# Performance work log

Measured on AMD Instinct MI355X. Metric: run time of the kernel, lower is better.

## Reference

```python
import jax, jax.numpy as jnp
import numpy as np

N, E, B = 10000, 100000, 64
IN_DIM, EDGE_DIM = 16, 8
HID = [32, 64]
OUT_DIM = 128
BN_EPS = 1e-5


def setup_inputs() -> dict:
    key = jax.random.key(0)
    ks = iter(jax.random.split(key, 32))
    inp = {}
    inp["x"] = jax.random.normal(next(ks), (N, IN_DIM), dtype=jnp.float32)
    inp["edge_index"] = jax.random.randint(next(ks), (2, E), 0, N, dtype=jnp.int64)
    inp["edge_attr"] = jax.random.normal(next(ks), (E, EDGE_DIM), dtype=jnp.float32)
    inp["batch"] = jnp.sort(jax.random.randint(next(ks), (N,), 0, B, dtype=jnp.int64))
    inp["edge_batch"] = jax.random.randint(next(ks), (E,), 0, B, dtype=jnp.int64)
    pre = IN_DIM
    for i, hd in enumerate(HID):
        s = 1.0 / np.sqrt(EDGE_DIM)
        inp[f"w_nn{i}"] = jax.random.uniform(next(ks), (pre * hd, EDGE_DIM), jnp.float32, -s, s)
        inp[f"b_nn{i}"] = jax.random.uniform(next(ks), (pre * hd,), jnp.float32, -s, s)
        inp[f"root{i}"] = jax.random.normal(next(ks), (pre, hd), dtype=jnp.float32) / np.sqrt(pre)
        inp[f"bias{i}"] = jnp.zeros((hd,), dtype=jnp.float32)
        inp[f"gamma{i}"] = jnp.ones((hd,), dtype=jnp.float32)
        inp[f"beta{i}"] = jnp.zeros((hd,), dtype=jnp.float32)
        pre = hd
    s = 1.0 / np.sqrt(pre)
    inp["s_w"] = jax.random.uniform(next(ks), (OUT_DIM, pre), jnp.float32, -s, s)
    inp["s_b"] = jax.random.uniform(next(ks), (OUT_DIM,), jnp.float32, -s, s)
    inp["t_w"] = jax.random.uniform(next(ks), (OUT_DIM, pre), jnp.float32, -s, s)
    inp["t_b"] = jax.random.uniform(next(ks), (OUT_DIM,), jnp.float32, -s, s)
    return inp


def _nnconv(x, edge_index, edge_attr, w_nn, b_nn, root, bias, out_dim):
    src, dst = edge_index[0], edge_index[1]
    # per-edge weight matrices [E, in_dim, out_dim]
    W = (edge_attr @ w_nn.T + b_nn).reshape(edge_attr.shape[0], -1, out_dim)
    msg = jnp.einsum('ei,eio->eo', x[src], W)  # gather + per-edge matmul
    agg = jax.ops.segment_sum(msg, dst, num_segments=N)  # scatter-add
    return agg + x @ root + bias


def _bn(x, gamma, beta):
    mu = jnp.mean(x, axis=0)
    var = jnp.mean((x - mu) ** 2, axis=0)  # biased var (torch BN training)
    return gamma * (x - mu) * jax.lax.rsqrt(var + BN_EPS) + beta


def reference(x, edge_index, edge_attr, batch, edge_batch,
              w_nn0, b_nn0, root0, bias0, gamma0, beta0,
              w_nn1, b_nn1, root1, bias1, gamma1, beta1,
              s_w, s_b, t_w, t_b):
    x = jax.nn.relu(_bn(_nnconv(x, edge_index, edge_attr, w_nn0, b_nn0, root0, bias0, HID[0]), gamma0, beta0))
    x = jax.nn.relu(_bn(_nnconv(x, edge_index, edge_attr, w_nn1, b_nn1, root1, bias1, HID[1]), gamma1, beta1))
    s_x = jnp.clip(x @ s_w.T + s_b, -30.0, 30.0)
    t_x = x @ t_w.T + t_b
    f_x = jax.nn.sigmoid(-s_x) * jnp.tanh(t_x)  # 1/(1+exp(s)) == sigmoid(-s)
    return jax.ops.segment_sum(f_x, batch, num_segments=B)
```

## Files before the change

### kernel.cpp

```cpp
#include <hip/hip_runtime.h>
#include <math.h>

#define NN 10000
#define NE 100000
#define BN_EPS 1e-5f

__global__ __launch_bounds__(256) void k_prep(
    const float* __restrict__ w0, const float* __restrict__ b0,
    const float* __restrict__ root0,
    const float* __restrict__ w1, const float* __restrict__ b1,
    const float* __restrict__ root1,
    const float* __restrict__ s_w, const float* __restrict__ t_w,
    float* __restrict__ wT0, float* __restrict__ wT1, float* __restrict__ wstT,
    float* __restrict__ st0, float* __restrict__ st1, float* __restrict__ out)
{
  int gid = blockIdx.x * 256 + threadIdx.x;
  int gsz = gridDim.x * 256;
  for (int idx = gid; idx < 16 * 320; idx += gsz) {
    int i = idx / 320, c = idx - i * 320;
    float v;
    if (c < 256)      v = w0[(i * 32 + (c & 31)) * 8 + (c >> 5)];
    else if (c < 288) v = b0[i * 32 + (c - 256)];
    else              v = root0[i * 32 + (c - 288)];
    wT0[idx] = v;
  }
  for (int idx = gid; idx < 32 * 640; idx += gsz) {
    int i = idx / 640, c = idx - i * 640;
    float v;
    if (c < 512)      v = w1[(i * 64 + (c & 63)) * 8 + (c >> 6)];
    else if (c < 576) v = b1[i * 64 + (c - 512)];
    else              v = root1[i * 64 + (c - 576)];
    wT1[idx] = v;
  }
  for (int idx = gid; idx < 64 * 256; idx += gsz) {
    int i = idx >> 8, o = idx & 255;
    wstT[idx] = (o < 128) ? s_w[o * 64 + i] : t_w[(o - 128) * 64 + i];
  }
  for (int idx = gid; idx < 64 * 128; idx += gsz) out[idx] = 0.f;
  if (gid < 64)  st0[gid] = 0.f;
  if (gid < 128) st1[gid] = 0.f;
}

__global__ __launch_bounds__(320) void k_node0(
    const float* __restrict__ x, const float* __restrict__ wT0,
    const float* __restrict__ bias0,
    float* __restrict__ G0, float* __restrict__ h0)
{
  int c = threadIdx.x;
  float wc[16];
#pragma unroll
  for (int i = 0; i < 16; ++i) wc[i] = wT0[i * 320 + c];
  float bi = (c >= 288) ? bias0[c - 288] : 0.f;

  int n0 = blockIdx.x * 20;
  for (int n = n0; n < n0 + 20; n += 2) {
    const float4* xa = (const float4*)(x + n * 16);
    float a0 = 0.f, a1 = 0.f;
#pragma unroll
    for (int q = 0; q < 4; ++q) {
      float4 v0 = xa[q], v1 = xa[q + 4];
      a0 = fmaf(v0.x, wc[4 * q + 0], a0); a1 = fmaf(v1.x, wc[4 * q + 0], a1);
      a0 = fmaf(v0.y, wc[4 * q + 1], a0); a1 = fmaf(v1.y, wc[4 * q + 1], a1);
      a0 = fmaf(v0.z, wc[4 * q + 2], a0); a1 = fmaf(v1.z, wc[4 * q + 2], a1);
      a0 = fmaf(v0.w, wc[4 * q + 3], a0); a1 = fmaf(v1.w, wc[4 * q + 3], a1);
    }
    if (c < 288) {
      G0[n * 288 + c]       = a0;
      G0[(n + 1) * 288 + c] = a1;
    } else {
      h0[n * 32 + (c - 288)]       = a0 + bi;
      h0[(n + 1) * 32 + (c - 288)] = a1 + bi;
    }
  }
}

__global__ __launch_bounds__(256) void k_edge0(
    const int* __restrict__ ei, const float* __restrict__ ea,
    const float* __restrict__ G0, float* __restrict__ h0)
{
  int tid = threadIdx.x;
  int e = blockIdx.x * 8 + (tid >> 5);
  if (e >= NE) return;
  int o = tid & 31;
  int src = ei[e], dst = ei[NE + e];
  const float* gr = G0 + src * 288;
  const float* er = ea + e * 8;
  float m = gr[256 + o];
#pragma unroll
  for (int k = 0; k < 8; ++k) m = fmaf(er[k], gr[k * 32 + o], m);
  unsafeAtomicAdd(&h0[dst * 32 + o], m);
}

template <int C>
__global__ __launch_bounds__(256) void k_stats(
    const float* __restrict__ h, float* __restrict__ st)
{
  const int RPB = 256 / C;
  int tid = threadIdx.x;
  int col = tid % C, rg = tid / C;
  float s1 = 0.f, s2 = 0.f;
  int step = gridDim.x * RPB;
  for (int n = blockIdx.x * RPB + rg; n < NN; n += step) {
    float v = h[n * C + col];
    s1 += v; s2 += v * v;
  }
  __shared__ float l1[256], l2[256];
  l1[tid] = s1; l2[tid] = s2;
  __syncthreads();
  if (tid < C) {
    for (int r = 1; r < RPB; ++r) { s1 += l1[r * C + tid]; s2 += l2[r * C + tid]; }
    unsafeAtomicAdd(&st[tid], s1);
    unsafeAtomicAdd(&st[C + tid], s2);
  }
}

__global__ __launch_bounds__(256) void k_x1(
    float* __restrict__ h0, const float* __restrict__ st0,
    const float* __restrict__ g0, const float* __restrict__ be0)
{
  __shared__ float sc[32], sh[32];
  int tid = threadIdx.x;
  if (tid < 32) {
    float mu  = st0[tid] * (1.0f / NN);
    float var = st0[32 + tid] * (1.0f / NN) - mu * mu;
    float s   = g0[tid] * rsqrtf(var + BN_EPS);
    sc[tid] = s;
    sh[tid] = be0[tid] - mu * s;
  }
  __syncthreads();
  const int NV = NN * 8;
  for (int i = blockIdx.x * 256 + tid; i < NV; i += gridDim.x * 256) {
    float4 v = ((const float4*)h0)[i];
    int c0 = (i * 4) & 31;
    v.x = fmaxf(fmaf(v.x, sc[c0],     sh[c0]),     0.f);
    v.y = fmaxf(fmaf(v.y, sc[c0 + 1], sh[c0 + 1]), 0.f);
    v.z = fmaxf(fmaf(v.z, sc[c0 + 2], sh[c0 + 2]), 0.f);
    v.w = fmaxf(fmaf(v.w, sc[c0 + 3], sh[c0 + 3]), 0.f);
    ((float4*)h0)[i] = v;
  }
}

__global__ __launch_bounds__(320) void k_node1(
    const float* __restrict__ x1, const float* __restrict__ wT1,
    const float* __restrict__ bias1,
    float* __restrict__ G1, float* __restrict__ h1)
{
  int t = threadIdx.x;
  float wa[32], wb[32];
#pragma unroll
  for (int i = 0; i < 32; ++i) {
    float2 w2 = *(const float2*)(wT1 + i * 640 + 2 * t);
    wa[i] = w2.x; wb[i] = w2.y;
  }
  float bia = 0.f, bib = 0.f;
  if (t >= 288) { bia = bias1[2 * (t - 288)]; bib = bias1[2 * (t - 288) + 1]; }

  int n0 = blockIdx.x * 20;
  for (int n = n0; n < n0 + 20; n += 2) {
    const float4* xa = (const float4*)(x1 + n * 32);
    float a00 = 0.f, a01 = 0.f, a10 = 0.f, a11 = 0.f;
#pragma unroll
    for (int q = 0; q < 8; ++q) {
      float4 v0 = xa[q], v1 = xa[q + 8];
      a00 = fmaf(v0.x, wa[4 * q + 0], a00); a01 = fmaf(v0.x, wb[4 * q + 0], a01);
      a00 = fmaf(v0.y, wa[4 * q + 1], a00); a01 = fmaf(v0.y, wb[4 * q + 1], a01);
      a00 = fmaf(v0.z, wa[4 * q + 2], a00); a01 = fmaf(v0.z, wb[4 * q + 2], a01);
      a00 = fmaf(v0.w, wa[4 * q + 3], a00); a01 = fmaf(v0.w, wb[4 * q + 3], a01);
      a10 = fmaf(v1.x, wa[4 * q + 0], a10); a11 = fmaf(v1.x, wb[4 * q + 0], a11);
      a10 = fmaf(v1.y, wa[4 * q + 1], a10); a11 = fmaf(v1.y, wb[4 * q + 1], a11);
      a10 = fmaf(v1.z, wa[4 * q + 2], a10); a11 = fmaf(v1.z, wb[4 * q + 2], a11);
      a10 = fmaf(v1.w, wa[4 * q + 3], a10); a11 = fmaf(v1.w, wb[4 * q + 3], a11);
    }
    if (t < 288) {
      *(float2*)(G1 + n * 576 + 2 * t)       = make_float2(a00, a01);
      *(float2*)(G1 + (n + 1) * 576 + 2 * t) = make_float2(a10, a11);
    } else {
      int o = 2 * (t - 288);
      *(float2*)(h1 + n * 64 + o)       = make_float2(a00 + bia, a01 + bib);
      *(float2*)(h1 + (n + 1) * 64 + o) = make_float2(a10 + bia, a11 + bib);
    }
  }
}

__global__ __launch_bounds__(256) void k_edge1(
    const int* __restrict__ ei, const float* __restrict__ ea,
    const float* __restrict__ G1, float* __restrict__ h1)
{
  int tid = threadIdx.x;
  int e = blockIdx.x * 4 + (tid >> 6);
  if (e >= NE) return;
  int o = tid & 63;
  int src = ei[e], dst = ei[NE + e];
  const float* gr = G1 + src * 576;
  const float* er = ea + e * 8;
  float m = gr[512 + o];
#pragma unroll
  for (int k = 0; k < 8; ++k) m = fmaf(er[k], gr[k * 64 + o], m);
  unsafeAtomicAdd(&h1[dst * 64 + o], m);
}

__global__ __launch_bounds__(256) void k_x2(
    float* __restrict__ h1, const float* __restrict__ st1,
    const float* __restrict__ g1, const float* __restrict__ be1)
{
  __shared__ float sc[64], sh[64];
  int tid = threadIdx.x;
  if (tid < 64) {
    float mu  = st1[tid] * (1.0f / NN);
    float var = st1[64 + tid] * (1.0f / NN) - mu * mu;
    float s   = g1[tid] * rsqrtf(var + BN_EPS);
    sc[tid] = s;
    sh[tid] = be1[tid] - mu * s;
  }
  __syncthreads();
  const int NV = NN * 16;
  for (int i = blockIdx.x * 256 + tid; i < NV; i += gridDim.x * 256) {
    float4 v = ((const float4*)h1)[i];
    int c0 = (i * 4) & 63;
    v.x = fmaxf(fmaf(v.x, sc[c0],     sh[c0]),     0.f);
    v.y = fmaxf(fmaf(v.y, sc[c0 + 1], sh[c0 + 1]), 0.f);
    v.z = fmaxf(fmaf(v.z, sc[c0 + 2], sh[c0 + 2]), 0.f);
    v.w = fmaxf(fmaf(v.w, sc[c0 + 3], sh[c0 + 3]), 0.f);
    ((float4*)h1)[i] = v;
  }
}

__global__ __launch_bounds__(256) void k_head(
    const float* __restrict__ x2, const float* __restrict__ wstT,
    const float* __restrict__ s_b, const float* __restrict__ t_b,
    const int* __restrict__ batch, float* __restrict__ out)
{
  int tid = threadIdx.x;
  int c = tid & 127, g = tid >> 7;
  int n0 = blockIdx.x * 40 + g * 20;
  int n1 = n0 + 20;
  if (n0 >= NN) return;
  if (n1 > NN) n1 = NN;

  float wsr[64], wtr[64];
#pragma unroll
  for (int k = 0; k < 64; ++k) {
    wsr[k] = wstT[k * 256 + c];
    wtr[k] = wstT[k * 256 + 128 + c];
  }
  float sb = s_b[c], tb = t_b[c];

  int bcur = batch[n0];
  float facc = 0.f;
  for (int n = n0; n < n1; ++n) {
    const float4* xr = (const float4*)(x2 + (size_t)n * 64);
    float as = 0.f, at = 0.f;
#pragma unroll
    for (int q = 0; q < 16; ++q) {
      float4 xv = xr[q];
      as = fmaf(xv.x, wsr[4 * q + 0], as); at = fmaf(xv.x, wtr[4 * q + 0], at);
      as = fmaf(xv.y, wsr[4 * q + 1], as); at = fmaf(xv.y, wtr[4 * q + 1], at);
      as = fmaf(xv.z, wsr[4 * q + 2], as); at = fmaf(xv.z, wtr[4 * q + 2], at);
      as = fmaf(xv.w, wsr[4 * q + 3], as); at = fmaf(xv.w, wtr[4 * q + 3], at);
    }
    float sv = fminf(30.f, fmaxf(-30.f, as + sb));
    float tv = at + tb;
    float f  = tanhf(tv) / (1.f + expf(sv));
    int b = batch[n];
    if (b != bcur) {
      unsafeAtomicAdd(&out[bcur * 128 + c], facc);
      bcur = b; facc = 0.f;
    }
    facc += f;
  }
  unsafeAtomicAdd(&out[bcur * 128 + c], facc);
}

extern "C" void kernel_launch(void* const* d_in, const int* in_sizes, int n_in,
                              void* d_out, int out_size, void* d_ws, size_t ws_size,
                              hipStream_t stream)
{
  const float* x     = (const float*)d_in[0];
  const int*   ei    = (const int*)d_in[1];
  const float* ea    = (const float*)d_in[2];
  const int*   batch = (const int*)d_in[3];
  const float* w0    = (const float*)d_in[5];
  const float* b0    = (const float*)d_in[6];
  const float* root0 = (const float*)d_in[7];
  const float* bias0 = (const float*)d_in[8];
  const float* g0    = (const float*)d_in[9];
  const float* be0   = (const float*)d_in[10];
  const float* w1    = (const float*)d_in[11];
  const float* b1    = (const float*)d_in[12];
  const float* root1 = (const float*)d_in[13];
  const float* bias1 = (const float*)d_in[14];
  const float* g1    = (const float*)d_in[15];
  const float* be1   = (const float*)d_in[16];
  const float* s_w   = (const float*)d_in[17];
  const float* s_b   = (const float*)d_in[18];
  const float* t_w   = (const float*)d_in[19];
  const float* t_b   = (const float*)d_in[20];
  float* out = (float*)d_out;

  float* ws   = (float*)d_ws;
  float* G0   = ws;  ws += 2880000;
  float* G1   = ws;  ws += 5760000;
  float* h0   = ws;  ws += 320000;
  float* h1   = ws;  ws += 640000;
  float* st0  = ws;  ws += 64;
  float* st1  = ws;  ws += 128;
  float* wstT = ws;  ws += 16384;
  float* wT0  = ws;  ws += 5120;
  float* wT1  = ws;  ws += 20480;

  hipLaunchKernelGGL(k_prep, dim3(64), dim3(256), 0, stream,
                     w0, b0, root0, w1, b1, root1, s_w, t_w,
                     wT0, wT1, wstT, st0, st1, out);
  hipLaunchKernelGGL(k_node0, dim3(500), dim3(320), 0, stream,
                     x, wT0, bias0, G0, h0);
  hipLaunchKernelGGL(k_edge0, dim3((NE + 7) / 8), dim3(256), 0, stream, ei, ea, G0, h0);
  hipLaunchKernelGGL(k_stats<32>, dim3(64), dim3(256), 0, stream, h0, st0);
  hipLaunchKernelGGL(k_x1, dim3(160), dim3(256), 0, stream, h0, st0, g0, be0);
  hipLaunchKernelGGL(k_node1, dim3(500), dim3(320), 0, stream,
                     h0, wT1, bias1, G1, h1);
  hipLaunchKernelGGL(k_edge1, dim3((NE + 3) / 4), dim3(256), 0, stream, ei, ea, G1, h1);
  hipLaunchKernelGGL(k_stats<64>, dim3(128), dim3(256), 0, stream, h1, st1);
  hipLaunchKernelGGL(k_x2, dim3(320), dim3(256), 0, stream, h1, st1, g1, be1);
  hipLaunchKernelGGL(k_head, dim3(250), dim3(256), 0, stream,
                     h1, wstT, s_b, t_b, batch, out);
}
```

Measured before the change: 210.5 us.

## Sort edges by source into CSR and gather G rows once per node

Adds a histogram, a single-block scan and a scatter pass that reorder edges by source node into a CSR layout with permuted edge attributes. Both edge kernels then loop per source node, loading the node's G row into registers once and reusing it across all of its outgoing edges, while still scattering to destinations with atomics. This is meant to cut the redundant gathers of large G rows (288 or 576 floats) that happened once per edge. In exchange it adds three preprocessing launches, including a serial single-block scan, plus a scatter of the edge attributes, and the per-node loops can be load-imbalanced across waves.

```diff
diff --git a/kernel.cpp b/kernel.cpp
--- a/kernel.cpp
+++ b/kernel.cpp
@@ -12,7 +12,8 @@
     const float* __restrict__ root1,
     const float* __restrict__ s_w, const float* __restrict__ t_w,
     float* __restrict__ wT0, float* __restrict__ wT1, float* __restrict__ wstT,
-    float* __restrict__ st0, float* __restrict__ st1, float* __restrict__ out)
+    float* __restrict__ st0, float* __restrict__ st1, float* __restrict__ out,
+    int* __restrict__ deg)
 {
   int gid = blockIdx.x * 256 + threadIdx.x;
   int gsz = gridDim.x * 256;
@@ -37,8 +38,58 @@
     wstT[idx] = (o < 128) ? s_w[o * 64 + i] : t_w[(o - 128) * 64 + i];
   }
   for (int idx = gid; idx < 64 * 128; idx += gsz) out[idx] = 0.f;
+  for (int idx = gid; idx < NN; idx += gsz) deg[idx] = 0;
   if (gid < 64)  st0[gid] = 0.f;
   if (gid < 128) st1[gid] = 0.f;
+}
+
+__global__ __launch_bounds__(256) void k_hist(
+    const int* __restrict__ ei, int* __restrict__ deg)
+{
+  int e = blockIdx.x * 256 + threadIdx.x;
+  if (e < NE) atomicAdd(&deg[ei[e]], 1);
+}
+
+__global__ __launch_bounds__(256) void k_scan(
+    const int* __restrict__ deg, int* __restrict__ row_ptr,
+    int* __restrict__ cursor)
+{
+  __shared__ int part[256];
+  int t = threadIdx.x;
+  int base = t * 40;
+  int s = 0;
+  for (int j = 0; j < 40; ++j) {
+    int idx = base + j;
+    if (idx < NN) s += deg[idx];
+  }
+  part[t] = s;
+  __syncthreads();
+  if (t == 0) {
+    int r = 0;
+    for (int i = 0; i < 256; ++i) { int v = part[i]; part[i] = r; r += v; }
+    row_ptr[NN] = r;
+  }
+  __syncthreads();
+  int r = part[t];
+  for (int j = 0; j < 40; ++j) {
+    int idx = base + j;
+    if (idx < NN) { row_ptr[idx] = r; cursor[idx] = r; r += deg[idx]; }
+  }
+}
+
+__global__ __launch_bounds__(256) void k_scatter(
+    const int* __restrict__ ei, const float* __restrict__ ea,
+    int* __restrict__ cursor, int* __restrict__ dstS, float* __restrict__ eaS)
+{
+  int e = blockIdx.x * 256 + threadIdx.x;
+  if (e >= NE) return;
+  int src = ei[e];
+  int p = atomicAdd(&cursor[src], 1);
+  dstS[p] = ei[NE + e];
+  const float4* ev = (const float4*)(ea + 8 * (size_t)e);
+  float4 a = ev[0], b = ev[1];
+  float4* ov = (float4*)(eaS + 8 * (size_t)p);
+  ov[0] = a; ov[1] = b;
 }
 
 __global__ __launch_bounds__(320) void k_node0(
@@ -74,21 +125,35 @@
   }
 }
 
-__global__ __launch_bounds__(256) void k_edge0(
-    const int* __restrict__ ei, const float* __restrict__ ea,
+__global__ __launch_bounds__(256) void k_edge0s(
+    const int* __restrict__ row_ptr, const int* __restrict__ dstS,
+    const float* __restrict__ eaS,
     const float* __restrict__ G0, float* __restrict__ h0)
 {
   int tid = threadIdx.x;
-  int e = blockIdx.x * 8 + (tid >> 5);
-  if (e >= NE) return;
-  int o = tid & 31;
-  int src = ei[e], dst = ei[NE + e];
-  const float* gr = G0 + src * 288;
-  const float* er = ea + e * 8;
-  float m = gr[256 + o];
-#pragma unroll
-  for (int k = 0; k < 8; ++k) m = fmaf(er[k], gr[k * 32 + o], m);
-  unsafeAtomicAdd(&h0[dst * 32 + o], m);
+  int lane = tid & 63;
+  int o = lane & 31, ph = lane >> 5;
+  int wv = blockIdx.x * 4 + (tid >> 6);
+  int nw = gridDim.x * 4;
+  for (int n = wv; n < NN; n += nw) {
+    const float* gr = G0 + (size_t)n * 288;
+    float g[8];
+#pragma unroll
+    for (int k = 0; k < 8; ++k) g[k] = gr[k * 32 + o];
+    float gb = gr[256 + o];
+    int p1 = row_ptr[n + 1];
+    for (int p = row_ptr[n] + ph; p < p1; p += 2) {
+      int dst = dstS[p];
+      const float4* ev = (const float4*)(eaS + 8 * (size_t)p);
+      float4 e0 = ev[0], e1 = ev[1];
+      float m = gb;
+      m = fmaf(e0.x, g[0], m); m = fmaf(e0.y, g[1], m);
+      m = fmaf(e0.z, g[2], m); m = fmaf(e0.w, g[3], m);
+      m = fmaf(e1.x, g[4], m); m = fmaf(e1.y, g[5], m);
+      m = fmaf(e1.z, g[6], m); m = fmaf(e1.w, g[7], m);
+      unsafeAtomicAdd(&h0[(size_t)dst * 32 + o], m);
+    }
+  }
 }
 
 template <int C>
@@ -182,21 +247,34 @@
   }
 }
 
-__global__ __launch_bounds__(256) void k_edge1(
-    const int* __restrict__ ei, const float* __restrict__ ea,
+__global__ __launch_bounds__(256) void k_edge1s(
+    const int* __restrict__ row_ptr, const int* __restrict__ dstS,
+    const float* __restrict__ eaS,
     const float* __restrict__ G1, float* __restrict__ h1)
 {
   int tid = threadIdx.x;
-  int e = blockIdx.x * 4 + (tid >> 6);
-  if (e >= NE) return;
   int o = tid & 63;
-  int src = ei[e], dst = ei[NE + e];
-  const float* gr = G1 + src * 576;
-  const float* er = ea + e * 8;
-  float m = gr[512 + o];
-#pragma unroll
-  for (int k = 0; k < 8; ++k) m = fmaf(er[k], gr[k * 64 + o], m);
-  unsafeAtomicAdd(&h1[dst * 64 + o], m);
+  int wv = blockIdx.x * 4 + (tid >> 6);
+  int nw = gridDim.x * 4;
+  for (int n = wv; n < NN; n += nw) {
+    const float* gr = G1 + (size_t)n * 576;
+    float g[8];
+#pragma unroll
+    for (int k = 0; k < 8; ++k) g[k] = gr[k * 64 + o];
+    float gb = gr[512 + o];
+    int p1 = row_ptr[n + 1];
+    for (int p = row_ptr[n]; p < p1; ++p) {
+      int dst = dstS[p];
+      const float4* ev = (const float4*)(eaS + 8 * (size_t)p);
+      float4 e0 = ev[0], e1 = ev[1];
+      float m = gb;
+      m = fmaf(e0.x, g[0], m); m = fmaf(e0.y, g[1], m);
+      m = fmaf(e0.z, g[2], m); m = fmaf(e0.w, g[3], m);
+      m = fmaf(e1.x, g[4], m); m = fmaf(e1.y, g[5], m);
+      m = fmaf(e1.z, g[6], m); m = fmaf(e1.w, g[7], m);
+      unsafeAtomicAdd(&h1[(size_t)dst * 64 + o], m);
+    }
+  }
 }
 
 __global__ __launch_bounds__(256) void k_x2(
@@ -307,18 +385,30 @@
   float* wstT = ws;  ws += 16384;
   float* wT0  = ws;  ws += 5120;
   float* wT1  = ws;  ws += 20480;
+  float* eaS  = ws;  ws += 800000;
+  int*   iw   = (int*)ws;
+  int* deg     = iw;  iw += NN;
+  int* row_ptr = iw;  iw += NN + 1;
+  int* cursor  = iw;  iw += NN;
+  int* dstS    = iw;  iw += NE;
 
   hipLaunchKernelGGL(k_prep, dim3(64), dim3(256), 0, stream,
                      w0, b0, root0, w1, b1, root1, s_w, t_w,
-                     wT0, wT1, wstT, st0, st1, out);
+                     wT0, wT1, wstT, st0, st1, out, deg);
+  hipLaunchKernelGGL(k_hist, dim3((NE + 255) / 256), dim3(256), 0, stream, ei, deg);
+  hipLaunchKernelGGL(k_scan, dim3(1), dim3(256), 0, stream, deg, row_ptr, cursor);
+  hipLaunchKernelGGL(k_scatter, dim3((NE + 255) / 256), dim3(256), 0, stream,
+                     ei, ea, cursor, dstS, eaS);
   hipLaunchKernelGGL(k_node0, dim3(500), dim3(320), 0, stream,
                      x, wT0, bias0, G0, h0);
-  hipLaunchKernelGGL(k_edge0, dim3((NE + 7) / 8), dim3(256), 0, stream, ei, ea, G0, h0);
+  hipLaunchKernelGGL(k_edge0s, dim3(625), dim3(256), 0, stream,
+                     row_ptr, dstS, eaS, G0, h0);
   hipLaunchKernelGGL(k_stats<32>, dim3(64), dim3(256), 0, stream, h0, st0);
   hipLaunchKernelGGL(k_x1, dim3(160), dim3(256), 0, stream, h0, st0, g0, be0);
   hipLaunchKernelGGL(k_node1, dim3(500), dim3(320), 0, stream,
                      h0, wT1, bias1, G1, h1);
-  hipLaunchKernelGGL(k_edge1, dim3((NE + 3) / 4), dim3(256), 0, stream, ei, ea, G1, h1);
+  hipLaunchKernelGGL(k_edge1s, dim3(625), dim3(256), 0, stream,
+                     row_ptr, dstS, eaS, G1, h1);
   hipLaunchKernelGGL(k_stats<64>, dim3(128), dim3(256), 0, stream, h1, st1);
   hipLaunchKernelGGL(k_x2, dim3(320), dim3(256), 0, stream, h1, st1, g1, be1);
   hipLaunchKernelGGL(k_head, dim3(250), dim3(256), 0, stream,
```

After: 258.8 us. +23.0%, slower.
